# Kernel tuning notes

Measured on AMD Instinct MI355X. Metric: run time of the kernel, lower is better.

The kernel has to match this reference:

```python
import jax, jax.numpy as jnp
import numpy as np
from jax import lax

B, N, D_MODEL = 2, 1024, 512
D_INNER, D_STATE, D_CONV, DT_RANK, RED = 1024, 16, 4, 32, 4
EPS = 1e-5


def setup_inputs() -> dict:
    key = jax.random.key(0)
    ks = jax.random.split(key, 40)
    f32 = jnp.float32
    inp = {}
    inp["I1"] = jax.random.normal(ks[0], (B, N, D_MODEL), f32)
    inp["I2"] = jax.random.normal(ks[1], (B, N, D_MODEL), f32)
    inp["norm1_w"] = jnp.ones((D_MODEL,), f32)
    inp["norm1_b"] = jnp.zeros((D_MODEL,), f32)
    inp["norm2_w"] = jnp.ones((D_MODEL,), f32)
    inp["norm2_b"] = jnp.zeros((D_MODEL,), f32)
    inp["se_w1"] = jax.random.normal(ks[2], (D_MODEL // RED, D_MODEL), f32) * 0.02
    inp["se_w2"] = jax.random.normal(ks[3], (D_MODEL, D_MODEL // RED), f32) * 0.02
    A = jnp.tile(jnp.arange(1, D_STATE + 1, dtype=f32), (D_INNER, 1))  # (d_inner, d_state)
    for i, base in ((1, 4), (2, 14)):
        p = f"m{i}_"
        inp[p + "in_w"] = jax.random.normal(ks[base + 0], (2 * D_INNER, D_MODEL), f32) * 0.02
        inp[p + "conv_w"] = jax.random.normal(ks[base + 1], (D_INNER, 1, D_CONV), f32) * 0.1
        inp[p + "conv_b"] = jnp.zeros((D_INNER,), f32)
        inp[p + "xproj_w"] = jax.random.normal(ks[base + 2], (DT_RANK + 2 * D_STATE, D_INNER), f32) * 0.02
        inp[p + "dt_w"] = jax.random.normal(ks[base + 3], (D_INNER, DT_RANK), f32) * 0.02
        inp[p + "dt_b"] = jax.random.normal(ks[base + 4], (D_INNER,), f32) * 0.1
        inp[p + "A_log"] = jnp.log(A)
        inp[p + "D"] = jnp.ones((D_INNER,), f32)
        inp[p + "out_w"] = jax.random.normal(ks[base + 5], (D_MODEL, D_INNER), f32) * 0.02
    return inp


def layernorm(x, w, b):
    mu = x.mean(-1, keepdims=True)
    var = ((x - mu) ** 2).mean(-1, keepdims=True)
    return (x - mu) * lax.rsqrt(var + EPS) * w + b


def silu(x):
    return x * jax.nn.sigmoid(x)


def mamba(x, in_w, conv_w, conv_b, xproj_w, dt_w, dt_b, A_log, Dp, out_w):
    # x: (B, L, d_model)
    b, L, _ = x.shape
    xz = x @ in_w.T                        # (B, L, 2*d_inner)
    xc, z = jnp.split(xz, 2, axis=-1)
    # depthwise causal conv1d over L
    xc = xc.transpose(0, 2, 1)             # (B, d_inner, L)
    xc = jnp.pad(xc, ((0, 0), (0, 0), (D_CONV - 1, 0)))
    xc = lax.conv_general_dilated(xc, conv_w, (1,), "VALID",
                                  dimension_numbers=("NCH", "OIH", "NCH"),
                                  feature_group_count=D_INNER)
    xc = silu(xc + conv_b[None, :, None]).transpose(0, 2, 1)  # (B, L, d_inner)
    x_dbl = xc @ xproj_w.T                 # (B, L, dt_rank + 2*d_state)
    dt, Bm, Cm = jnp.split(x_dbl, [DT_RANK, DT_RANK + D_STATE], axis=-1)
    dt = jax.nn.softplus(dt @ dt_w.T + dt_b)      # (B, L, d_inner)
    A = -jnp.exp(A_log)                           # (d_inner, d_state)
    dA = jnp.exp(dt[..., None] * A)               # (B, L, d_inner, d_state)
    dBu = dt[..., None] * Bm[:, :, None, :] * xc[..., None]

    def step(h, inputs):
        dA_t, dBu_t, C_t = inputs
        h = dA_t * h + dBu_t                      # (B, d_inner, d_state)
        y = jnp.einsum("bds,bs->bd", h, C_t)
        return h, y

    h0 = jnp.zeros((b, D_INNER, D_STATE), x.dtype)
    _, ys = lax.scan(step, h0, (dA.transpose(1, 0, 2, 3),
                                dBu.transpose(1, 0, 2, 3),
                                Cm.transpose(1, 0, 2)))
    y = ys.transpose(1, 0, 2)                     # (B, L, d_inner)
    y = y + xc * Dp
    y = y * silu(z)
    return y @ out_w.T                            # (B, L, d_model)


def se_block(x, w1, w2):
    y = x.mean(axis=1)                            # (B, C)
    y = jax.nn.sigmoid(jax.nn.relu(y @ w1.T) @ w2.T)
    return x * y[:, None, :]


def channel_exchange(x1, x2):
    c = x1.shape[-1]
    mask = (jnp.arange(c) % 2 == 0)               # swap channels where c % p == 0
    return jnp.where(mask, x2, x1), jnp.where(mask, x1, x2)


def reference(I1, I2, norm1_w, norm1_b, norm2_w, norm2_b, se_w1, se_w2,
              m1_in_w, m1_conv_w, m1_conv_b, m1_xproj_w, m1_dt_w, m1_dt_b, m1_A_log, m1_D, m1_out_w,
              m2_in_w, m2_conv_w, m2_conv_b, m2_xproj_w, m2_dt_w, m2_dt_b, m2_A_log, m2_D, m2_out_w):
    I1n = layernorm(I1, norm1_w, norm1_b)
    I2n = layernorm(I2, norm2_w, norm2_b)
    s1, s2 = channel_exchange(I1n, I2n)
    s1 = se_block(s1, se_w1, se_w2)
    s2 = se_block(s2, se_w1, se_w2)
    o1 = mamba(s1, m1_in_w, m1_conv_w, m1_conv_b, m1_xproj_w, m1_dt_w, m1_dt_b, m1_A_log, m1_D, m1_out_w) + I1
    o2 = mamba(s2, m2_in_w, m2_conv_w, m2_conv_b, m2_xproj_w, m2_dt_w, m2_dt_b, m2_A_log, m2_D, m2_out_w) + I2
    return (o1, o2)
```

## Files before the change

### kernel.cpp

```cpp
#include <hip/hip_runtime.h>
#include <hip/hip_bf16.h>

constexpr int kB   = 2;
constexpr int kN   = 1024;
constexpr int kDM  = 512;
constexpr int kDI  = 1024;
constexpr int kDS  = 16;
constexpr int kDTR = 32;
constexpr int kNC  = 32;
constexpr int kCL  = 32;

typedef __attribute__((ext_vector_type(8))) __bf16 bf16x8;
typedef __attribute__((ext_vector_type(4))) __bf16 bf16x4;
typedef __attribute__((ext_vector_type(4))) float  f32x4;

#define GLD16(g, l) __builtin_amdgcn_global_load_lds( \
    (const __attribute__((address_space(1))) void*)(g), \
    (__attribute__((address_space(3))) void*)(l), 16, 0, 0)

__device__ __forceinline__ float sigmoidf_(float x) { return 1.f / (1.f + __expf(-x)); }
__device__ __forceinline__ float sum4(float4 a) { return a.x + a.y + a.z + a.w; }
__device__ __forceinline__ float dot4(float4 a) { return a.x*a.x + a.y*a.y + a.z*a.z + a.w*a.w; }
__device__ __forceinline__ float4 nrm4(float4 x, float mu, float rs, float4 w, float4 b) {
    return make_float4((x.x-mu)*rs*w.x + b.x, (x.y-mu)*rs*w.y + b.y,
                       (x.z-mu)*rs*w.z + b.z, (x.w-mu)*rs*w.w + b.w);
}
__device__ __forceinline__ bf16x4 tob4(float4 v) {
    return (bf16x4){(__bf16)v.x, (__bf16)v.y, (__bf16)v.z, (__bf16)v.w};
}

__launch_bounds__(256)
__global__ void ln_exchange_k(const float* __restrict__ I1, const float* __restrict__ I2,
                              const float* __restrict__ w1, const float* __restrict__ b1,
                              const float* __restrict__ w2, const float* __restrict__ b2,
                              __bf16* __restrict__ s1b, __bf16* __restrict__ s2b,
                              float* __restrict__ partial)
{
    int w    = threadIdx.x >> 6;
    int row  = blockIdx.x * 4 + w;
    int lane = threadIdx.x & 63;
    const float4* p1 = reinterpret_cast<const float4*>(I1 + (size_t)row * kDM);
    const float4* p2 = reinterpret_cast<const float4*>(I2 + (size_t)row * kDM);
    float4 xa1 = p1[lane], xb1 = p1[lane + 64];
    float4 xa2 = p2[lane], xb2 = p2[lane + 64];
    float su1 = sum4(xa1) + sum4(xb1), sq1 = dot4(xa1) + dot4(xb1);
    float su2 = sum4(xa2) + sum4(xb2), sq2 = dot4(xa2) + dot4(xb2);
    #pragma unroll
    for (int m = 32; m; m >>= 1) {
        su1 += __shfl_xor(su1, m, 64); sq1 += __shfl_xor(sq1, m, 64);
        su2 += __shfl_xor(su2, m, 64); sq2 += __shfl_xor(sq2, m, 64);
    }
    float mu1 = su1 * (1.f / kDM), v1 = sq1 * (1.f / kDM) - mu1 * mu1;
    float mu2 = su2 * (1.f / kDM), v2 = sq2 * (1.f / kDM) - mu2 * mu2;
    float rs1 = rsqrtf(v1 + 1e-5f), rs2 = rsqrtf(v2 + 1e-5f);
    const float4* W1 = reinterpret_cast<const float4*>(w1);
    const float4* B1 = reinterpret_cast<const float4*>(b1);
    const float4* W2 = reinterpret_cast<const float4*>(w2);
    const float4* B2 = reinterpret_cast<const float4*>(b2);
    float4 w1a = W1[lane], w1b = W1[lane+64], b1a = B1[lane], b1b = B1[lane+64];
    float4 w2a = W2[lane], w2b = W2[lane+64], b2a = B2[lane], b2b = B2[lane+64];
    float4 n1a = nrm4(xa1, mu1, rs1, w1a, b1a), n1b = nrm4(xb1, mu1, rs1, w1b, b1b);
    float4 n2a = nrm4(xa2, mu2, rs2, w2a, b2a), n2b = nrm4(xb2, mu2, rs2, w2b, b2b);
    float4 o1a = make_float4(n2a.x, n1a.y, n2a.z, n1a.w);
    float4 o2a = make_float4(n1a.x, n2a.y, n1a.z, n2a.w);
    float4 o1b = make_float4(n2b.x, n1b.y, n2b.z, n1b.w);
    float4 o2b = make_float4(n1b.x, n2b.y, n1b.z, n2b.w);
    bf16x4* q1 = reinterpret_cast<bf16x4*>(s1b + (size_t)row * kDM);
    bf16x4* q2 = reinterpret_cast<bf16x4*>(s2b + (size_t)row * kDM);
    q1[lane] = tob4(o1a); q1[lane + 64] = tob4(o1b);
    q2[lane] = tob4(o2a); q2[lane + 64] = tob4(o2b);

    __shared__ float lp[2][4][kDM];
    int c0 = lane * 4, c1 = 256 + lane * 4;
    lp[0][w][c0+0] = o1a.x; lp[0][w][c0+1] = o1a.y; lp[0][w][c0+2] = o1a.z; lp[0][w][c0+3] = o1a.w;
    lp[0][w][c1+0] = o1b.x; lp[0][w][c1+1] = o1b.y; lp[0][w][c1+2] = o1b.z; lp[0][w][c1+3] = o1b.w;
    lp[1][w][c0+0] = o2a.x; lp[1][w][c0+1] = o2a.y; lp[1][w][c0+2] = o2a.z; lp[1][w][c0+3] = o2a.w;
    lp[1][w][c1+0] = o2b.x; lp[1][w][c1+1] = o2b.y; lp[1][w][c1+2] = o2b.z; lp[1][w][c1+3] = o2b.w;
    __syncthreads();
    for (int c = threadIdx.x; c < kDM; c += 256) {
        partial[((size_t)0 * 512 + blockIdx.x) * kDM + c] =
            lp[0][0][c] + lp[0][1][c] + lp[0][2][c] + lp[0][3][c];
        partial[((size_t)1 * 512 + blockIdx.x) * kDM + c] =
            lp[1][0][c] + lp[1][1][c] + lp[1][2][c] + lp[1][3][c];
    }
}

__launch_bounds__(256)
__global__ void col_red_k(const float* __restrict__ partial, float* __restrict__ partial2)
{
    int x = blockIdx.x;
    int g = x & 31;
    int b = (x >> 5) & 1;
    int t = x >> 6;
    const float* src = partial + ((size_t)t * 512 + b * 256 + g * 8) * kDM;
    float* dst = partial2 + ((size_t)((t * 2 + b) * 32 + g)) * kDM;
    for (int c = threadIdx.x; c < kDM; c += 256) {
        float acc = 0.f;
        #pragma unroll
        for (int i = 0; i < 8; ++i) acc += src[(size_t)i * kDM + c];
        dst[c] = acc;
    }
}

__launch_bounds__(256)
__global__ void se_mlp_k(const float* __restrict__ partial2,
                         const float* __restrict__ w1, const float* __restrict__ w2,
                         float* __restrict__ scl1, float* __restrict__ scl2)
{
    int t = blockIdx.x >> 1, b = blockIdx.x & 1;
    float* scl = (t ? scl2 : scl1) + b * kDM;
    __shared__ float m[kDM];
    __shared__ float hid[128];
    const float* pb = partial2 + (size_t)((t * 2 + b) * 32) * kDM;
    for (int c = threadIdx.x; c < kDM; c += 256) {
        float acc = 0.f;
        #pragma unroll
        for (int i = 0; i < 32; ++i) acc += pb[(size_t)i * kDM + c];
        m[c] = acc * (1.f / kN);
    }
    __syncthreads();
    if (threadIdx.x < 128) {
        int j = threadIdx.x;
        const float4* wv = reinterpret_cast<const float4*>(w1 + (size_t)j * kDM);
        float acc = 0.f;
        #pragma unroll 4
        for (int c = 0; c < kDM; c += 4) {
            float4 w = wv[c >> 2];
            acc = fmaf(m[c+0], w.x, acc);
            acc = fmaf(m[c+1], w.y, acc);
            acc = fmaf(m[c+2], w.z, acc);
            acc = fmaf(m[c+3], w.w, acc);
        }
        hid[j] = fmaxf(acc, 0.f);
    }
    __syncthreads();
    for (int c = threadIdx.x; c < kDM; c += 256) {
        const float4* wv = reinterpret_cast<const float4*>(w2 + (size_t)c * 128);
        float a2 = 0.f;
        #pragma unroll 4
        for (int k = 0; k < 128; k += 4) {
            float4 w = wv[k >> 2];
            a2 = fmaf(hid[k+0], w.x, a2);
            a2 = fmaf(hid[k+1], w.y, a2);
            a2 = fmaf(hid[k+2], w.z, a2);
            a2 = fmaf(hid[k+3], w.w, a2);
        }
        scl[c] = sigmoidf_(a2);
    }
}

__launch_bounds__(256)
__global__ void scale_cvt_all_k(const __bf16* __restrict__ s1b, const __bf16* __restrict__ s2b,
                                const float* __restrict__ scl1, const float* __restrict__ scl2,
                                __bf16* __restrict__ sA0, __bf16* __restrict__ sA1,
                                const float* __restrict__ in0, __bf16* __restrict__ win0,
                                const float* __restrict__ xp0, __bf16* __restrict__ wxp0,
                                const float* __restrict__ ow0, __bf16* __restrict__ wow0,
                                const float* __restrict__ in1, __bf16* __restrict__ win1,
                                const float* __restrict__ xp1, __bf16* __restrict__ wxp1,
                                const float* __restrict__ ow1, __bf16* __restrict__ wow1)
{
    int gidx = blockIdx.x * 256 + threadIdx.x;
    if (gidx < 262144) {
        int mam = gidx >> 17;
        int i = gidx & 131071;
        const __bf16* s = mam ? s2b : s1b;
        const float* scl = mam ? scl2 : scl1;
        __bf16* out = mam ? sA1 : sA0;
        bf16x8 v = reinterpret_cast<const bf16x8*>(s)[i];
        int cg = (i & 63) * 2;
        int row = i >> 6;
        int b = row >> 10;
        const float4* sp = reinterpret_cast<const float4*>(scl + b * kDM);
        float4 sa = sp[cg], sb = sp[cg + 1];
        bf16x8 o;
        o[0] = (__bf16)((float)v[0] * sa.x); o[1] = (__bf16)((float)v[1] * sa.y);
        o[2] = (__bf16)((float)v[2] * sa.z); o[3] = (__bf16)((float)v[3] * sa.w);
        o[4] = (__bf16)((float)v[4] * sb.x); o[5] = (__bf16)((float)v[5] * sb.y);
        o[6] = (__bf16)((float)v[6] * sb.z); o[7] = (__bf16)((float)v[7] * sb.w);
        reinterpret_cast<bf16x8*>(out)[i] = o;
        return;
    }
    int idx = gidx - 262144;
    const float* src; __bf16* dst; int base;
    if (idx < 262144)      { src = in0; dst = win0; base = 0; }
    else if (idx < 278528) { src = xp0; dst = wxp0; base = 262144; }
    else if (idx < 409600) { src = ow0; dst = wow0; base = 278528; }
    else if (idx < 671744) { src = in1; dst = win1; base = 409600; }
    else if (idx < 688128) { src = xp1; dst = wxp1; base = 671744; }
    else                   { src = ow1; dst = wow1; base = 688128; }
    int i = idx - base;
    float4 v = reinterpret_cast<const float4*>(src)[i];
    reinterpret_cast<bf16x4*>(dst)[i] = tob4(v);
}

template<typename OT>
__global__ __launch_bounds__(256) void gemm_lds_k(
    const __bf16* __restrict__ A0, const __bf16* __restrict__ A1,
    const __bf16* __restrict__ B0, const __bf16* __restrict__ B1,
    OT* __restrict__ C0, OT* __restrict__ C1,
    int M, int N, int K)
{
    __shared__ __bf16 lA[128 * 32];
    __shared__ __bf16 lB[128 * 32];
    int tiles_n = N >> 7, tiles_m = M >> 7;
    int per = tiles_m * tiles_n;
    int blk = blockIdx.x;
    int mam = blk >= per;
    if (mam) blk -= per;
    const __bf16* A  = mam ? A1 : A0;
    const __bf16* Bw = mam ? B1 : B0;
    OT*           C  = mam ? C1 : C0;
    int tm = blk / tiles_n, tn = blk % tiles_n;
    int tid = threadIdx.x;
    int w = tid >> 6, lane = tid & 63;
    int wr = w >> 1, wc = w & 1;

    f32x4 acc[4][4];
    #pragma unroll
    for (int i = 0; i < 4; ++i)
        #pragma unroll
        for (int j = 0; j < 4; ++j)
            acc[i][j] = (f32x4){0.f, 0.f, 0.f, 0.f};

    const __bf16* Abase = A  + (size_t)tm * 128 * K;
    const __bf16* Bbase = Bw + (size_t)tn * 128 * K;
    int srow = (lane >> 2);
    int skk  = (lane & 3) * 8;

    for (int k0 = 0; k0 < K; k0 += 32) {
        #pragma unroll
        for (int r = 0; r < 2; ++r) {
            int seg = r * 4 + w;
            int row = seg * 16 + srow;
            GLD16(Abase + (size_t)row * K + k0 + skk, &lA[seg * 512]);
            GLD16(Bbase + (size_t)row * K + k0 + skk, &lB[seg * 512]);
        }
        __syncthreads();
        bf16x8 af[4], bfr[4];
        #pragma unroll
        for (int i = 0; i < 4; ++i)
            af[i] = *reinterpret_cast<const bf16x8*>(
                &lA[(wr * 64 + i * 16 + (lane & 15)) * 32 + (lane >> 4) * 8]);
        #pragma unroll
        for (int j = 0; j < 4; ++j)
            bfr[j] = *reinterpret_cast<const bf16x8*>(
                &lB[(wc * 64 + j * 16 + (lane & 15)) * 32 + (lane >> 4) * 8]);
        #pragma unroll
        for (int i = 0; i < 4; ++i)
            #pragma unroll
            for (int j = 0; j < 4; ++j)
                acc[i][j] = __builtin_amdgcn_mfma_f32_16x16x32_bf16(af[i], bfr[j], acc[i][j], 0, 0, 0);
        __syncthreads();
    }
    int row0 = tm * 128 + wr * 64 + ((lane >> 4) << 2);
    int col0 = tn * 128 + wc * 64 + (lane & 15);
    #pragma unroll
    for (int i = 0; i < 4; ++i)
        #pragma unroll
        for (int j = 0; j < 4; ++j)
            #pragma unroll
            for (int rr = 0; rr < 4; ++rr)
                C[(size_t)(row0 + i * 16 + rr) * N + col0 + j * 16] = (OT)acc[i][j][rr];
}

template<int WM16, int WN16, bool ADD_RES, typename OT>
__global__ __launch_bounds__(256) void gemm_bt2(
    const __bf16* __restrict__ A0, const __bf16* __restrict__ A1,
    const __bf16* __restrict__ B0, const __bf16* __restrict__ B1,
    const float* __restrict__ R0, const float* __restrict__ R1,
    OT* __restrict__ C0, OT* __restrict__ C1,
    int M, int N, int K)
{
    constexpr int WM = 16 * WM16, WN = 16 * WN16;
    int tiles_n = N / WN;
    int tiles_m = M / WM;
    int per = tiles_m * tiles_n;
    int wave = blockIdx.x * (blockDim.x >> 6) + (threadIdx.x >> 6);
    int mam = wave >= per;
    if (mam) wave -= per;
    const __bf16* A  = mam ? A1 : A0;
    const __bf16* Bw = mam ? B1 : B0;
    const float*  R  = mam ? R1 : R0;
    OT*           C  = mam ? C1 : C0;
    int tm = wave / tiles_n, tn = wave % tiles_n;
    int lane = threadIdx.x & 63;
    int r = lane & 15;
    int ko = (lane >> 4) * 8;
    const __bf16* Abase = A  + (size_t)(tm * WM + r) * K + ko;
    const __bf16* Bbase = Bw + (size_t)(tn * WN + r) * K + ko;
    f32x4 acc[WM16][WN16];
    #pragma unroll
    for (int i = 0; i < WM16; ++i)
        #pragma unroll
        for (int j = 0; j < WN16; ++j)
            acc[i][j] = (f32x4){0.f, 0.f, 0.f, 0.f};
    for (int k0 = 0; k0 < K; k0 += 32) {
        bf16x8 a[WM16], b[WN16];
        #pragma unroll
        for (int i = 0; i < WM16; ++i)
            a[i] = *reinterpret_cast<const bf16x8*>(Abase + (size_t)i * 16 * K + k0);
        #pragma unroll
        for (int j = 0; j < WN16; ++j)
            b[j] = *reinterpret_cast<const bf16x8*>(Bbase + (size_t)j * 16 * K + k0);
        #pragma unroll
        for (int i = 0; i < WM16; ++i)
            #pragma unroll
            for (int j = 0; j < WN16; ++j)
                acc[i][j] = __builtin_amdgcn_mfma_f32_16x16x32_bf16(a[i], b[j], acc[i][j], 0, 0, 0);
    }
    int row0 = tm * WM + ((lane >> 4) << 2);
    int col0 = tn * WN + (lane & 15);
    #pragma unroll
    for (int i = 0; i < WM16; ++i)
        #pragma unroll
        for (int j = 0; j < WN16; ++j)
            #pragma unroll
            for (int rr = 0; rr < 4; ++rr) {
                size_t idx = (size_t)(row0 + i * 16 + rr) * N + col0 + j * 16;
                float v = acc[i][j][rr];
                if (ADD_RES) v += R[idx];
                C[idx] = (OT)v;
            }
}

__launch_bounds__(256)
__global__ void conv_silu_k(const __bf16* __restrict__ xz0, const __bf16* __restrict__ xz1,
                            const float* __restrict__ cw0, const float* __restrict__ cw1,
                            const float* __restrict__ cb0, const float* __restrict__ cb1,
                            __bf16* __restrict__ xcb0, __bf16* __restrict__ xcb1)
{
    int gidx = blockIdx.x * 256 + threadIdx.x;
    int mam = gidx >> 21;
    int idx = gidx & ((1 << 21) - 1);
    const __bf16* xz = mam ? xz1 : xz0;
    const float* cw = mam ? cw1 : cw0;
    const float* cb = mam ? cb1 : cb0;
    __bf16* xcb = mam ? xcb1 : xcb0;
    int d = idx & (kDI - 1);
    int n = (idx >> 10) & (kN - 1);
    int b = idx >> 20;
    const __bf16* base = xz + (size_t)(b << 10) * (2 * kDI) + d;
    float acc = cb[d];
    #pragma unroll
    for (int j = 0; j < 4; ++j) {
        int nn = n - 3 + j;
        if (nn >= 0) acc = fmaf((float)base[(size_t)nn * (2 * kDI)], cw[d * 4 + j], acc);
    }
    float o = acc * sigmoidf_(acc);
    xcb[idx] = (__bf16)o;
}

__device__ __forceinline__ size_t ph_idx(int bm, int c, int s, int d) {
    return (((size_t)bm * kNC + c) * kDS + s) * kDI + d;
}

__device__ __forceinline__ float dt_inline(const float4* __restrict__ xdr, int t,
                                           const float* __restrict__ wdt, float bias)
{
    float acc = bias;
    #pragma unroll
    for (int q = 0; q < 8; ++q) {
        float4 v = xdr[t * 16 + q];
        acc = fmaf(v.x, wdt[q*4+0], acc);
        acc = fmaf(v.y, wdt[q*4+1], acc);
        acc = fmaf(v.z, wdt[q*4+2], acc);
        acc = fmaf(v.w, wdt[q*4+3], acc);
    }
    return acc > 15.f ? acc : log1pf(__expf(acc));
}

__launch_bounds__(256)
__global__ void scan_p1(const __bf16* __restrict__ xc_0, const __bf16* __restrict__ xc_1,
                        const float* __restrict__ xd_0, const float* __restrict__ xd_1,
                        const float* __restrict__ dtw0, const float* __restrict__ dtw1,
                        const float* __restrict__ dtb0, const float* __restrict__ dtb1,
                        const float* __restrict__ Al_0, const float* __restrict__ Al_1,
                        __bf16* __restrict__ Pbuf, __bf16* __restrict__ Hbuf)
{
    int bid = blockIdx.x;
    int dgrp = bid & 3;
    int c    = (bid >> 2) & (kNC - 1);
    int b    = (bid >> 7) & 1;
    int mam  = bid >> 8;
    int d    = dgrp * 256 + threadIdx.x;
    int bm   = mam * 2 + b;
    const __bf16* xcp = mam ? xc_1 : xc_0;
    const float* xdp = mam ? xd_1 : xd_0;
    const float* Alp = mam ? Al_1 : Al_0;
    const float* dtw = mam ? dtw1 : dtw0;
    float bias = (mam ? dtb1 : dtb0)[d];

    float wdt[kDTR];
    {
        const float4* wv = reinterpret_cast<const float4*>(dtw + (size_t)d * kDTR);
        #pragma unroll
        for (int q = 0; q < 8; ++q) {
            float4 v = wv[q];
            wdt[q*4+0] = v.x; wdt[q*4+1] = v.y; wdt[q*4+2] = v.z; wdt[q*4+3] = v.w;
        }
    }
    float a[kDS], h[kDS], P[kDS];
    {
        const float4* Av = reinterpret_cast<const float4*>(Alp + d * kDS);
        #pragma unroll
        for (int q = 0; q < 4; ++q) {
            float4 v = Av[q];
            a[q*4+0] = -__expf(v.x); a[q*4+1] = -__expf(v.y);
            a[q*4+2] = -__expf(v.z); a[q*4+3] = -__expf(v.w);
        }
    }
    #pragma unroll
    for (int s = 0; s < kDS; ++s) { h[s] = 0.f; P[s] = 1.f; }

    int t0 = c * kCL;
    const __bf16* xcr = xcp + ((size_t)b * kN + t0) * kDI + d;
    const float4* xdr = reinterpret_cast<const float4*>(xdp + ((size_t)b * kN + t0) * 64);

    for (int t = 0; t < kCL; ++t) {
        float dtv = dt_inline(xdr, t, wdt, bias);
        float xcv = (float)xcr[(size_t)t * kDI];
        float4 B0 = xdr[t * 16 + 8],  B1 = xdr[t * 16 + 9];
        float4 B2 = xdr[t * 16 + 10], B3 = xdr[t * 16 + 11];
        float Bv[kDS] = {B0.x,B0.y,B0.z,B0.w, B1.x,B1.y,B1.z,B1.w,
                         B2.x,B2.y,B2.z,B2.w, B3.x,B3.y,B3.z,B3.w};
        float dtxc = dtv * xcv;
        #pragma unroll
        for (int s = 0; s < kDS; ++s) {
            float dA = __expf(dtv * a[s]);
            P[s] *= dA;
            h[s] = fmaf(dA, h[s], dtxc * Bv[s]);
        }
    }
    #pragma unroll
    for (int s = 0; s < kDS; ++s) {
        Pbuf[ph_idx(bm, c, s, d)] = (__bf16)P[s];
        Hbuf[ph_idx(bm, c, s, d)] = (__bf16)h[s];
    }
}

__launch_bounds__(256)
__global__ void scan_p2(const __bf16* __restrict__ Pbuf, const __bf16* __restrict__ Hbuf,
                        __bf16* __restrict__ Init)
{
    int i = blockIdx.x * 256 + threadIdx.x;
    int d = i & (kDI - 1);
    int s = (i >> 10) & 15;
    int bm = i >> 14;
    float h = 0.f;
    #pragma unroll 4
    for (int c = 0; c < kNC; ++c) {
        size_t o = ph_idx(bm, c, s, d);
        Init[o] = (__bf16)h;
        h = fmaf((float)Pbuf[o], h, (float)Hbuf[o]);
    }
}

__launch_bounds__(256)
__global__ void scan_p3(const __bf16* __restrict__ xc_0, const __bf16* __restrict__ xc_1,
                        const __bf16* __restrict__ xz_0, const __bf16* __restrict__ xz_1,
                        const float* __restrict__ xd_0, const float* __restrict__ xd_1,
                        const float* __restrict__ dtw0, const float* __restrict__ dtw1,
                        const float* __restrict__ dtb0, const float* __restrict__ dtb1,
                        const float* __restrict__ Al_0, const float* __restrict__ Al_1,
                        const float* __restrict__ Dp_0, const float* __restrict__ Dp_1,
                        const __bf16* __restrict__ Init,
                        __bf16* __restrict__ yg_0, __bf16* __restrict__ yg_1)
{
    int bid = blockIdx.x;
    int dgrp = bid & 3;
    int c    = (bid >> 2) & (kNC - 1);
    int b    = (bid >> 7) & 1;
    int mam  = bid >> 8;
    int d    = dgrp * 256 + threadIdx.x;
    int bm   = mam * 2 + b;
    const __bf16* xcp = mam ? xc_1 : xc_0;
    const __bf16* xzp = mam ? xz_1 : xz_0;
    const float* xdp = mam ? xd_1 : xd_0;
    const float* Alp = mam ? Al_1 : Al_0;
    const float* Dpp = mam ? Dp_1 : Dp_0;
    const float* dtw = mam ? dtw1 : dtw0;
    float bias = (mam ? dtb1 : dtb0)[d];
    __bf16* ygp = mam ? yg_1 : yg_0;

    float wdt[kDTR];
    {
        const float4* wv = reinterpret_cast<const float4*>(dtw + (size_t)d * kDTR);
        #pragma unroll
        for (int q = 0; q < 8; ++q) {
            float4 v = wv[q];
            wdt[q*4+0] = v.x; wdt[q*4+1] = v.y; wdt[q*4+2] = v.z; wdt[q*4+3] = v.w;
        }
    }
    float a[kDS], h[kDS];
    {
        const float4* Av = reinterpret_cast<const float4*>(Alp + d * kDS);
        #pragma unroll
        for (int q = 0; q < 4; ++q) {
            float4 v = Av[q];
            a[q*4+0] = -__expf(v.x); a[q*4+1] = -__expf(v.y);
            a[q*4+2] = -__expf(v.z); a[q*4+3] = -__expf(v.w);
        }
    }
    #pragma unroll
    for (int s = 0; s < kDS; ++s) h[s] = (float)Init[ph_idx(bm, c, s, d)];
    float Dd = Dpp[d];

    int t0 = c * kCL;
    const __bf16* xcr = xcp + ((size_t)b * kN + t0) * kDI + d;
    const __bf16* zr  = xzp + ((size_t)b * kN + t0) * 2 * kDI + kDI + d;
    const float4* xdr = reinterpret_cast<const float4*>(xdp + ((size_t)b * kN + t0) * 64);
    __bf16* yr = ygp + ((size_t)b * kN + t0) * kDI + d;

    for (int t = 0; t < kCL; ++t) {
        float dtv = dt_inline(xdr, t, wdt, bias);
        float xcv = (float)xcr[(size_t)t * kDI];
        float zv  = (float)zr[(size_t)t * 2 * kDI];
        float4 B0 = xdr[t * 16 + 8],  B1 = xdr[t * 16 + 9];
        float4 B2 = xdr[t * 16 + 10], B3 = xdr[t * 16 + 11];
        float4 C0 = xdr[t * 16 + 12], C1 = xdr[t * 16 + 13];
        float4 C2 = xdr[t * 16 + 14], C3 = xdr[t * 16 + 15];
        float Bv[kDS] = {B0.x,B0.y,B0.z,B0.w, B1.x,B1.y,B1.z,B1.w,
                         B2.x,B2.y,B2.z,B2.w, B3.x,B3.y,B3.z,B3.w};
        float Cv[kDS] = {C0.x,C0.y,C0.z,C0.w, C1.x,C1.y,C1.z,C1.w,
                         C2.x,C2.y,C2.z,C2.w, C3.x,C3.y,C3.z,C3.w};
        float dtxc = dtv * xcv;
        float acc0 = 0.f, acc1 = 0.f, acc2 = 0.f, acc3 = 0.f;
        #pragma unroll
        for (int s = 0; s < kDS; s += 4) {
            float dA0 = __expf(dtv * a[s+0]);
            float dA1 = __expf(dtv * a[s+1]);
            float dA2 = __expf(dtv * a[s+2]);
            float dA3 = __expf(dtv * a[s+3]);
            h[s+0] = fmaf(dA0, h[s+0], dtxc * Bv[s+0]);
            h[s+1] = fmaf(dA1, h[s+1], dtxc * Bv[s+1]);
            h[s+2] = fmaf(dA2, h[s+2], dtxc * Bv[s+2]);
            h[s+3] = fmaf(dA3, h[s+3], dtxc * Bv[s+3]);
            acc0 = fmaf(h[s+0], Cv[s+0], acc0);
            acc1 = fmaf(h[s+1], Cv[s+1], acc1);
            acc2 = fmaf(h[s+2], Cv[s+2], acc2);
            acc3 = fmaf(h[s+3], Cv[s+3], acc3);
        }
        float y = (acc0 + acc1) + (acc2 + acc3) + xcv * Dd;
        yr[(size_t)t * kDI] = (__bf16)(y * zv * sigmoidf_(zv));
    }
}

extern "C" void kernel_launch(void* const* d_in, const int* in_sizes, int n_in,
                              void* d_out, int out_size, void* d_ws, size_t ws_size,
                              hipStream_t stream)
{
    (void)in_sizes; (void)n_in; (void)out_size; (void)ws_size;
    const float* I1  = (const float*)d_in[0];
    const float* I2  = (const float*)d_in[1];
    const float* n1w = (const float*)d_in[2];
    const float* n1b = (const float*)d_in[3];
    const float* n2w = (const float*)d_in[4];
    const float* n2b = (const float*)d_in[5];
    const float* sew1 = (const float*)d_in[6];
    const float* sew2 = (const float*)d_in[7];
    const float* in_w[2]   = {(const float*)d_in[8],  (const float*)d_in[17]};
    const float* conv_w[2] = {(const float*)d_in[9],  (const float*)d_in[18]};
    const float* conv_b[2] = {(const float*)d_in[10], (const float*)d_in[19]};
    const float* xp_w[2]   = {(const float*)d_in[11], (const float*)d_in[20]};
    const float* dt_w[2]   = {(const float*)d_in[12], (const float*)d_in[21]};
    const float* dt_b[2]   = {(const float*)d_in[13], (const float*)d_in[22]};
    const float* A_log[2]  = {(const float*)d_in[14], (const float*)d_in[23]};
    const float* Dp[2]     = {(const float*)d_in[15], (const float*)d_in[24]};
    const float* out_w[2]  = {(const float*)d_in[16], (const float*)d_in[25]};

    char* base = (char*)d_ws;
    size_t off = 0;
    auto alloc = [&](size_t bytes) -> char* {
        char* p = base + off;
        off = (off + bytes + 255) & ~(size_t)255;
        return p;
    };
    __bf16*  s1b  = (__bf16*)alloc((size_t)2 << 20);
    __bf16*  s2b  = (__bf16*)alloc((size_t)2 << 20);
    float*   partial  = (float*)alloc((size_t)2 * 512 * kDM * 4);
    float*   partial2 = (float*)alloc((size_t)128 * kDM * 4);
    float*   scl1 = (float*)alloc(1024 * 4);
    float*   scl2 = (float*)alloc(1024 * 4);
    __bf16*  sA[2]    = {(__bf16*)alloc((size_t)2 << 20), (__bf16*)alloc((size_t)2 << 20)};
    __bf16*  w_in[2]  = {(__bf16*)alloc((size_t)2 << 20), (__bf16*)alloc((size_t)2 << 20)};
    __bf16*  w_xp[2]  = {(__bf16*)alloc((size_t)128 << 10), (__bf16*)alloc((size_t)128 << 10)};
    __bf16*  w_out[2] = {(__bf16*)alloc((size_t)1 << 20), (__bf16*)alloc((size_t)1 << 20)};
    __bf16*  xzb[2] = {(__bf16*)alloc((size_t)8 << 20), (__bf16*)alloc((size_t)8 << 20)};
    __bf16*  xcb[2] = {(__bf16*)alloc((size_t)4 << 20), (__bf16*)alloc((size_t)4 << 20)};
    float*   xd[2]  = {(float*)alloc((size_t)512 << 10), (float*)alloc((size_t)512 << 10)};
    __bf16*  yg[2]  = {(__bf16*)alloc((size_t)4 << 20), (__bf16*)alloc((size_t)4 << 20)};
    __bf16*  Pbuf   = (__bf16*)alloc((size_t)4 << 20);
    __bf16*  Hbuf   = (__bf16*)alloc((size_t)4 << 20);
    __bf16*  Init   = (__bf16*)alloc((size_t)4 << 20);
    float* o1 = (float*)d_out;
    float* o2 = o1 + (size_t)kB * kN * kDM;

    ln_exchange_k<<<512, 256, 0, stream>>>(I1, I2, n1w, n1b, n2w, n2b, s1b, s2b, partial);
    col_red_k<<<128, 256, 0, stream>>>(partial, partial2);
    se_mlp_k<<<4, 256, 0, stream>>>(partial2, sew1, sew2, scl1, scl2);
    scale_cvt_all_k<<<4224, 256, 0, stream>>>(s1b, s2b, scl1, scl2, sA[0], sA[1],
                                              in_w[0], w_in[0], xp_w[0], w_xp[0],
                                              out_w[0], w_out[0],
                                              in_w[1], w_in[1], xp_w[1], w_xp[1],
                                              out_w[1], w_out[1]);
    gemm_lds_k<__bf16><<<512, 256, 0, stream>>>(
        sA[0], sA[1], w_in[0], w_in[1], xzb[0], xzb[1], kB * kN, 2 * kDI, kDM);
    conv_silu_k<<<16384, 256, 0, stream>>>(xzb[0], xzb[1], conv_w[0], conv_w[1],
                                           conv_b[0], conv_b[1], xcb[0], xcb[1]);
    gemm_bt2<1, 2, false, float><<<128, 256, 0, stream>>>(
        xcb[0], xcb[1], w_xp[0], w_xp[1], nullptr, nullptr, xd[0], xd[1],
        kB * kN, 64, kDI);
    scan_p1<<<512, 256, 0, stream>>>(xcb[0], xcb[1], xd[0], xd[1],
                                     dt_w[0], dt_w[1], dt_b[0], dt_b[1],
                                     A_log[0], A_log[1], Pbuf, Hbuf);
    scan_p2<<<256, 256, 0, stream>>>(Pbuf, Hbuf, Init);
    scan_p3<<<512, 256, 0, stream>>>(xcb[0], xcb[1], xzb[0], xzb[1], xd[0], xd[1],
                                     dt_w[0], dt_w[1], dt_b[0], dt_b[1],
                                     A_log[0], A_log[1], Dp[0], Dp[1],
                                     Init, yg[0], yg[1]);
    gemm_bt2<2, 2, true, float><<<512, 256, 0, stream>>>(
        yg[0], yg[1], w_out[0], w_out[1], I1, I2, o1, o2, kB * kN, kDM, kDI);
}
```

Measured before the change: 206.0 us.

## Precompute dt softplus once, vectorize conv, halve scan chunk length

Moves the dt projection and softplus out of both scan passes into a dedicated kernel that writes dt once as bf16. This removes duplicated per-step 32-wide dot products and transcendental work in scan_p1 and scan_p3. The change also vectorizes the causal conv to eight channels per thread and computes each chunk's decay product as exp of the summed dt instead of a running product. It doubles the number of scan chunks to raise parallelism, at the cost of larger P/H/Init buffers, a longer sequential scan_p2, and extra bf16 rounding of dt.

```diff
diff --git a/kernel.cpp b/kernel.cpp
--- a/kernel.cpp
+++ b/kernel.cpp
@@ -7,8 +7,8 @@
 constexpr int kDI  = 1024;
 constexpr int kDS  = 16;
 constexpr int kDTR = 32;
-constexpr int kNC  = 32;
-constexpr int kCL  = 32;
+constexpr int kNC  = 64;
+constexpr int kCL  = 16;
 
 typedef __attribute__((ext_vector_type(8))) __bf16 bf16x8;
 typedef __attribute__((ext_vector_type(4))) __bf16 bf16x4;
@@ -331,76 +331,114 @@
                             __bf16* __restrict__ xcb0, __bf16* __restrict__ xcb1)
 {
     int gidx = blockIdx.x * 256 + threadIdx.x;
-    int mam = gidx >> 21;
-    int idx = gidx & ((1 << 21) - 1);
+    int mam = gidx >> 18;
+    int idx = gidx & 262143;
+    int d8 = idx & 127;
+    int n  = (idx >> 7) & 1023;
+    int b  = idx >> 17;
     const __bf16* xz = mam ? xz1 : xz0;
     const float* cw = mam ? cw1 : cw0;
     const float* cb = mam ? cb1 : cb0;
     __bf16* xcb = mam ? xcb1 : xcb0;
-    int d = idx & (kDI - 1);
-    int n = (idx >> 10) & (kN - 1);
-    int b = idx >> 20;
-    const __bf16* base = xz + (size_t)(b << 10) * (2 * kDI) + d;
-    float acc = cb[d];
+    int d0 = d8 * 8;
+    float4 wv[8];
+    #pragma unroll
+    for (int i = 0; i < 8; ++i)
+        wv[i] = reinterpret_cast<const float4*>(cw)[d0 + i];
+    float accs[8];
+    {
+        float4 cb0v = reinterpret_cast<const float4*>(cb + d0)[0];
+        float4 cb1v = reinterpret_cast<const float4*>(cb + d0)[1];
+        accs[0]=cb0v.x; accs[1]=cb0v.y; accs[2]=cb0v.z; accs[3]=cb0v.w;
+        accs[4]=cb1v.x; accs[5]=cb1v.y; accs[6]=cb1v.z; accs[7]=cb1v.w;
+    }
+    const __bf16* base = xz + (size_t)(b << 10) * (2 * kDI) + d0;
     #pragma unroll
     for (int j = 0; j < 4; ++j) {
         int nn = n - 3 + j;
-        if (nn >= 0) acc = fmaf((float)base[(size_t)nn * (2 * kDI)], cw[d * 4 + j], acc);
-    }
-    float o = acc * sigmoidf_(acc);
-    xcb[idx] = (__bf16)o;
+        if (nn >= 0) {
+            bf16x8 v = *reinterpret_cast<const bf16x8*>(base + (size_t)nn * (2 * kDI));
+            accs[0] = fmaf((float)v[0], wv[0].x * (j==0) + wv[0].y * (j==1) + wv[0].z * (j==2) + wv[0].w * (j==3), accs[0]);
+            #pragma unroll
+            for (int i = 1; i < 8; ++i) {
+                float tap = (j==0) ? wv[i].x : (j==1) ? wv[i].y : (j==2) ? wv[i].z : wv[i].w;
+                accs[i] = fmaf((float)v[i], tap, accs[i]);
+            }
+        }
+    }
+    bf16x8 o;
+    #pragma unroll
+    for (int i = 0; i < 8; ++i) {
+        float x = accs[i];
+        o[i] = (__bf16)(x * sigmoidf_(x));
+    }
+    *reinterpret_cast<bf16x8*>(xcb + ((size_t)(b << 10) + n) * kDI + d0) = o;
+}
+
+__launch_bounds__(256)
+__global__ void dt_softplus_k(const float* __restrict__ xd0, const float* __restrict__ xd1,
+                              const float* __restrict__ dtw0, const float* __restrict__ dtw1,
+                              const float* __restrict__ dtb0, const float* __restrict__ dtb1,
+                              __bf16* __restrict__ out0, __bf16* __restrict__ out1)
+{
+    int idx = blockIdx.x * 256 + threadIdx.x;
+    int d = idx & (kDI - 1);
+    int rest = idx >> 10;
+    int mblk = rest & 511;
+    int mam = rest >> 9;
+    const float* xd  = mam ? xd1 : xd0;
+    const float* dtw = mam ? dtw1 : dtw0;
+    float bias = (mam ? dtb1 : dtb0)[d];
+    __bf16* dtout = mam ? out1 : out0;
+    float w[kDTR];
+    const float4* wv = reinterpret_cast<const float4*>(dtw + (size_t)d * kDTR);
+    #pragma unroll
+    for (int q = 0; q < 8; ++q) {
+        float4 v = wv[q];
+        w[q*4+0] = v.x; w[q*4+1] = v.y; w[q*4+2] = v.z; w[q*4+3] = v.w;
+    }
+    #pragma unroll
+    for (int mi = 0; mi < 4; ++mi) {
+        int m = mblk * 4 + mi;
+        const float4* xv = reinterpret_cast<const float4*>(xd + (size_t)m * 64);
+        float acc = bias;
+        #pragma unroll
+        for (int q = 0; q < 8; ++q) {
+            float4 v = xv[q];
+            acc = fmaf(v.x, w[q*4+0], acc);
+            acc = fmaf(v.y, w[q*4+1], acc);
+            acc = fmaf(v.z, w[q*4+2], acc);
+            acc = fmaf(v.w, w[q*4+3], acc);
+        }
+        float sp = acc > 15.f ? acc : log1pf(__expf(acc));
+        dtout[(size_t)m * kDI + d] = (__bf16)sp;
+    }
 }
 
 __device__ __forceinline__ size_t ph_idx(int bm, int c, int s, int d) {
     return (((size_t)bm * kNC + c) * kDS + s) * kDI + d;
 }
 
-__device__ __forceinline__ float dt_inline(const float4* __restrict__ xdr, int t,
-                                           const float* __restrict__ wdt, float bias)
-{
-    float acc = bias;
-    #pragma unroll
-    for (int q = 0; q < 8; ++q) {
-        float4 v = xdr[t * 16 + q];
-        acc = fmaf(v.x, wdt[q*4+0], acc);
-        acc = fmaf(v.y, wdt[q*4+1], acc);
-        acc = fmaf(v.z, wdt[q*4+2], acc);
-        acc = fmaf(v.w, wdt[q*4+3], acc);
-    }
-    return acc > 15.f ? acc : log1pf(__expf(acc));
-}
-
-__launch_bounds__(256)
-__global__ void scan_p1(const __bf16* __restrict__ xc_0, const __bf16* __restrict__ xc_1,
+__launch_bounds__(256)
+__global__ void scan_p1(const __bf16* __restrict__ dt_0, const __bf16* __restrict__ dt_1,
+                        const __bf16* __restrict__ xc_0, const __bf16* __restrict__ xc_1,
                         const float* __restrict__ xd_0, const float* __restrict__ xd_1,
-                        const float* __restrict__ dtw0, const float* __restrict__ dtw1,
-                        const float* __restrict__ dtb0, const float* __restrict__ dtb1,
                         const float* __restrict__ Al_0, const float* __restrict__ Al_1,
                         __bf16* __restrict__ Pbuf, __bf16* __restrict__ Hbuf)
 {
     int bid = blockIdx.x;
     int dgrp = bid & 3;
     int c    = (bid >> 2) & (kNC - 1);
-    int b    = (bid >> 7) & 1;
-    int mam  = bid >> 8;
+    int b    = (bid >> 8) & 1;
+    int mam  = bid >> 9;
     int d    = dgrp * 256 + threadIdx.x;
     int bm   = mam * 2 + b;
+    const __bf16* dtp = mam ? dt_1 : dt_0;
     const __bf16* xcp = mam ? xc_1 : xc_0;
     const float* xdp = mam ? xd_1 : xd_0;
     const float* Alp = mam ? Al_1 : Al_0;
-    const float* dtw = mam ? dtw1 : dtw0;
-    float bias = (mam ? dtb1 : dtb0)[d];
-
-    float wdt[kDTR];
-    {
-        const float4* wv = reinterpret_cast<const float4*>(dtw + (size_t)d * kDTR);
-        #pragma unroll
-        for (int q = 0; q < 8; ++q) {
-            float4 v = wv[q];
-            wdt[q*4+0] = v.x; wdt[q*4+1] = v.y; wdt[q*4+2] = v.z; wdt[q*4+3] = v.w;
-        }
-    }
-    float a[kDS], h[kDS], P[kDS];
+
+    float a[kDS], h[kDS];
     {
         const float4* Av = reinterpret_cast<const float4*>(Alp + d * kDS);
         #pragma unroll
@@ -411,30 +449,32 @@
         }
     }
     #pragma unroll
-    for (int s = 0; s < kDS; ++s) { h[s] = 0.f; P[s] = 1.f; }
+    for (int s = 0; s < kDS; ++s) h[s] = 0.f;
+    float dtsum = 0.f;
 
     int t0 = c * kCL;
+    const __bf16* dtr = dtp + ((size_t)b * kN + t0) * kDI + d;
     const __bf16* xcr = xcp + ((size_t)b * kN + t0) * kDI + d;
     const float4* xdr = reinterpret_cast<const float4*>(xdp + ((size_t)b * kN + t0) * 64);
 
     for (int t = 0; t < kCL; ++t) {
-        float dtv = dt_inline(xdr, t, wdt, bias);
+        float dtv = (float)dtr[(size_t)t * kDI];
         float xcv = (float)xcr[(size_t)t * kDI];
         float4 B0 = xdr[t * 16 + 8],  B1 = xdr[t * 16 + 9];
         float4 B2 = xdr[t * 16 + 10], B3 = xdr[t * 16 + 11];
         float Bv[kDS] = {B0.x,B0.y,B0.z,B0.w, B1.x,B1.y,B1.z,B1.w,
                          B2.x,B2.y,B2.z,B2.w, B3.x,B3.y,B3.z,B3.w};
+        dtsum += dtv;
         float dtxc = dtv * xcv;
         #pragma unroll
         for (int s = 0; s < kDS; ++s) {
             float dA = __expf(dtv * a[s]);
-            P[s] *= dA;
             h[s] = fmaf(dA, h[s], dtxc * Bv[s]);
         }
     }
     #pragma unroll
     for (int s = 0; s < kDS; ++s) {
-        Pbuf[ph_idx(bm, c, s, d)] = (__bf16)P[s];
+        Pbuf[ph_idx(bm, c, s, d)] = (__bf16)__expf(dtsum * a[s]);
         Hbuf[ph_idx(bm, c, s, d)] = (__bf16)h[s];
     }
 }
@@ -457,11 +497,10 @@
 }
 
 __launch_bounds__(256)
-__global__ void scan_p3(const __bf16* __restrict__ xc_0, const __bf16* __restrict__ xc_1,
+__global__ void scan_p3(const __bf16* __restrict__ dt_0, const __bf16* __restrict__ dt_1,
+                        const __bf16* __restrict__ xc_0, const __bf16* __restrict__ xc_1,
                         const __bf16* __restrict__ xz_0, const __bf16* __restrict__ xz_1,
                         const float* __restrict__ xd_0, const float* __restrict__ xd_1,
-                        const float* __restrict__ dtw0, const float* __restrict__ dtw1,
-                        const float* __restrict__ dtb0, const float* __restrict__ dtb1,
                         const float* __restrict__ Al_0, const float* __restrict__ Al_1,
                         const float* __restrict__ Dp_0, const float* __restrict__ Dp_1,
                         const __bf16* __restrict__ Init,
@@ -470,28 +509,18 @@
     int bid = blockIdx.x;
     int dgrp = bid & 3;
     int c    = (bid >> 2) & (kNC - 1);
-    int b    = (bid >> 7) & 1;
-    int mam  = bid >> 8;
+    int b    = (bid >> 8) & 1;
+    int mam  = bid >> 9;
     int d    = dgrp * 256 + threadIdx.x;
     int bm   = mam * 2 + b;
+    const __bf16* dtp = mam ? dt_1 : dt_0;
     const __bf16* xcp = mam ? xc_1 : xc_0;
     const __bf16* xzp = mam ? xz_1 : xz_0;
     const float* xdp = mam ? xd_1 : xd_0;
     const float* Alp = mam ? Al_1 : Al_0;
     const float* Dpp = mam ? Dp_1 : Dp_0;
-    const float* dtw = mam ? dtw1 : dtw0;
-    float bias = (mam ? dtb1 : dtb0)[d];
     __bf16* ygp = mam ? yg_1 : yg_0;
 
-    float wdt[kDTR];
-    {
-        const float4* wv = reinterpret_cast<const float4*>(dtw + (size_t)d * kDTR);
-        #pragma unroll
-        for (int q = 0; q < 8; ++q) {
-            float4 v = wv[q];
-            wdt[q*4+0] = v.x; wdt[q*4+1] = v.y; wdt[q*4+2] = v.z; wdt[q*4+3] = v.w;
-        }
-    }
     float a[kDS], h[kDS];
     {
         const float4* Av = reinterpret_cast<const float4*>(Alp + d * kDS);
@@ -507,13 +536,14 @@
     float Dd = Dpp[d];
 
     int t0 = c * kCL;
+    const __bf16* dtr = dtp + ((size_t)b * kN + t0) * kDI + d;
     const __bf16* xcr = xcp + ((size_t)b * kN + t0) * kDI + d;
     const __bf16* zr  = xzp + ((size_t)b * kN + t0) * 2 * kDI + kDI + d;
     const float4* xdr = reinterpret_cast<const float4*>(xdp + ((size_t)b * kN + t0) * 64);
     __bf16* yr = ygp + ((size_t)b * kN + t0) * kDI + d;
 
     for (int t = 0; t < kCL; ++t) {
-        float dtv = dt_inline(xdr, t, wdt, bias);
+        float dtv = (float)dtr[(size_t)t * kDI];
         float xcv = (float)xcr[(size_t)t * kDI];
         float zv  = (float)zr[(size_t)t * 2 * kDI];
         float4 B0 = xdr[t * 16 + 8],  B1 = xdr[t * 16 + 9];
@@ -589,10 +619,11 @@
     __bf16*  xzb[2] = {(__bf16*)alloc((size_t)8 << 20), (__bf16*)alloc((size_t)8 << 20)};
     __bf16*  xcb[2] = {(__bf16*)alloc((size_t)4 << 20), (__bf16*)alloc((size_t)4 << 20)};
     float*   xd[2]  = {(float*)alloc((size_t)512 << 10), (float*)alloc((size_t)512 << 10)};
+    __bf16*  dtb[2] = {(__bf16*)alloc((size_t)4 << 20), (__bf16*)alloc((size_t)4 << 20)};
     __bf16*  yg[2]  = {(__bf16*)alloc((size_t)4 << 20), (__bf16*)alloc((size_t)4 << 20)};
-    __bf16*  Pbuf   = (__bf16*)alloc((size_t)4 << 20);
-    __bf16*  Hbuf   = (__bf16*)alloc((size_t)4 << 20);
-    __bf16*  Init   = (__bf16*)alloc((size_t)4 << 20);
+    __bf16*  Pbuf   = (__bf16*)alloc((size_t)8 << 20);
+    __bf16*  Hbuf   = (__bf16*)alloc((size_t)8 << 20);
+    __bf16*  Init   = (__bf16*)alloc((size_t)8 << 20);
     float* o1 = (float*)d_out;
     float* o2 = o1 + (size_t)kB * kN * kDM;
 
@@ -606,19 +637,19 @@
                                               out_w[1], w_out[1]);
     gemm_lds_k<__bf16><<<512, 256, 0, stream>>>(
         sA[0], sA[1], w_in[0], w_in[1], xzb[0], xzb[1], kB * kN, 2 * kDI, kDM);
-    conv_silu_k<<<16384, 256, 0, stream>>>(xzb[0], xzb[1], conv_w[0], conv_w[1],
-                                           conv_b[0], conv_b[1], xcb[0], xcb[1]);
+    conv_silu_k<<<2048, 256, 0, stream>>>(xzb[0], xzb[1], conv_w[0], conv_w[1],
+                                          conv_b[0], conv_b[1], xcb[0], xcb[1]);
     gemm_bt2<1, 2, false, float><<<128, 256, 0, stream>>>(
         xcb[0], xcb[1], w_xp[0], w_xp[1], nullptr, nullptr, xd[0], xd[1],
         kB * kN, 64, kDI);
-    scan_p1<<<512, 256, 0, stream>>>(xcb[0], xcb[1], xd[0], xd[1],
-                                     dt_w[0], dt_w[1], dt_b[0], dt_b[1],
-                                     A_log[0], A_log[1], Pbuf, Hbuf);
+    dt_softplus_k<<<4096, 256, 0, stream>>>(xd[0], xd[1], dt_w[0], dt_w[1],
+                                            dt_b[0], dt_b[1], dtb[0], dtb[1]);
+    scan_p1<<<1024, 256, 0, stream>>>(dtb[0], dtb[1], xcb[0], xcb[1], xd[0], xd[1],
+                                      A_log[0], A_log[1], Pbuf, Hbuf);
     scan_p2<<<256, 256, 0, stream>>>(Pbuf, Hbuf, Init);
-    scan_p3<<<512, 256, 0, stream>>>(xcb[0], xcb[1], xzb[0], xzb[1], xd[0], xd[1],
-                                     dt_w[0], dt_w[1], dt_b[0], dt_b[1],
-                                     A_log[0], A_log[1], Dp[0], Dp[1],
-                                     Init, yg[0], yg[1]);
+    scan_p3<<<1024, 256, 0, stream>>>(dtb[0], dtb[1], xcb[0], xcb[1], xzb[0], xzb[1],
+                                      xd[0], xd[1], A_log[0], A_log[1], Dp[0], Dp[1],
+                                      Init, yg[0], yg[1]);
     gemm_bt2<2, 2, true, float><<<512, 256, 0, stream>>>(
         yg[0], yg[1], w_out[0], w_out[1], I1, I2, o1, o2, kB * kN, kDM, kDI);
 }
```

Result: faster. 200.8 us (-2.5%).
